# Kernel optimization log

Measured on AMD Instinct MI355X. Metric: run time of the kernel, lower is better.

Reference implementation:

```python
import jax, jax.numpy as jnp
import numpy as np

D_MODEL = 1024
N_HEADS = 16
HEAD_DIM = 64
INNER = N_HEADS * HEAD_DIM
D_FF = 4096


def ln_novar(x, w, b):
    # mean-only 'layernorm' (no variance division), per original LayerNormNoVar
    u = jnp.mean(x, axis=-1, keepdims=True)
    return w * (x - u) + b


def setup_inputs() -> dict:
    key = jax.random.key(0)
    ks = jax.random.split(key, 12)
    s = lambda k, shape, scale: jax.random.normal(k, shape, dtype=jnp.float32) * scale
    inp = {
        "src": s(ks[0], (4, 2048, D_MODEL), 1.0),
        "pre_norm_w": jnp.ones((D_MODEL,), jnp.float32),
        "pre_norm_b": jnp.zeros((D_MODEL,), jnp.float32),
        "wq": s(ks[1], (D_MODEL, INNER), 0.02),
        "wk": s(ks[2], (D_MODEL, INNER), 0.02),
        "wv": s(ks[3], (D_MODEL, INNER), 0.02),
        "w_proj": s(ks[4], (INNER, D_MODEL), 0.02),
        "b_proj": jnp.zeros((D_MODEL,), jnp.float32),
        "norm1_w": jnp.ones((D_MODEL,), jnp.float32),
        "norm1_b": jnp.zeros((D_MODEL,), jnp.float32),
        "w1": s(ks[5], (D_MODEL, D_FF), 0.02),
        "b1": jnp.zeros((D_FF,), jnp.float32),
        "w2": s(ks[6], (D_FF, D_MODEL), 0.02),
        "b2": jnp.zeros((D_MODEL,), jnp.float32),
    }
    return inp


def reference(src, pre_norm_w, pre_norm_b, wq, wk, wv, w_proj, b_proj,
              norm1_w, norm1_b, w1, b1, w2, b2):
    B, N, _ = src.shape
    scale = HEAD_DIM ** -0.5
    x = ln_novar(src, pre_norm_w, pre_norm_b)
    q = (x @ wq).reshape(B, N, N_HEADS, HEAD_DIM)
    k = (x @ wk).reshape(B, N, N_HEADS, HEAD_DIM)
    v = (x @ wv).reshape(B, N, N_HEADS, HEAD_DIM)
    attn = jnp.einsum('bqhd,bkhd->bhqk', q, k) * scale
    attn = jax.nn.softmax(attn, axis=-1)
    o = jnp.einsum('bhqk,bkhd->bqhd', attn, v).reshape(B, N, INNER)
    o = o @ w_proj + b_proj
    src = src + o
    src = ln_novar(src, norm1_w, norm1_b)
    ff = jax.nn.relu(src @ w1 + b1) @ w2 + b2
    return src + ff
```

## Files before the change

### kernel.cpp

```cpp
#include <hip/hip_runtime.h>
#include <hip/hip_bf16.h>
#include <stdint.h>

typedef __hip_bfloat16 bf16;
typedef float f32x4 __attribute__((ext_vector_type(4)));
typedef float f32x16 __attribute__((ext_vector_type(16)));
typedef short v8s __attribute__((ext_vector_type(8)));
typedef __bf16 v8bf __attribute__((ext_vector_type(8)));
typedef unsigned int v4u __attribute__((ext_vector_type(4)));
typedef unsigned int u32;

static constexpr int MROWS = 8192;
static constexpr int DM    = 1024;
static constexpr int DFF   = 4096;
static constexpr int SEQ   = 2048;

__device__ __forceinline__ f32x4 mfma16(v8s a, v8s b, f32x4 c) {
  return __builtin_amdgcn_mfma_f32_16x16x32_bf16(
      __builtin_bit_cast(v8bf, a), __builtin_bit_cast(v8bf, b), c, 0, 0, 0);
}
__device__ __forceinline__ f32x16 mfma32(v8s a, v8s b, f32x16 c) {
  return __builtin_amdgcn_mfma_f32_32x32x16_bf16(
      __builtin_bit_cast(v8bf, a), __builtin_bit_cast(v8bf, b), c, 0, 0, 0);
}

__device__ __forceinline__ void gload_lds16(const void* g, void* l) {
  __builtin_amdgcn_global_load_lds(
      (const __attribute__((address_space(1))) void*)g,
      (__attribute__((address_space(3))) void*)l, 16, 0, 0);
}

__device__ __forceinline__ u32 cvtpk_bf16(float a, float b) {
  u32 r;
  asm("v_cvt_pk_bf16_f32 %0, %1, %2" : "=v"(r) : "v"(a), "v"(b));
  return r;
}
__device__ __forceinline__ void pl32swap(u32& x, u32& y) {
  asm volatile("v_permlane32_swap_b32 %0, %1" : "+v"(x), "+v"(y));
}
__device__ __forceinline__ float fast_exp2(float x) {
  float r;
  asm("v_exp_f32 %0, %1" : "=v"(r) : "v"(x));
  return r;
}

__global__ __launch_bounds__(256) void transpose_cast(
    const float* __restrict__ W, bf16* __restrict__ WT, int K, int N) {
  __shared__ float tile[32][33];
  const int c0 = blockIdx.x * 32;
  const int r0 = blockIdx.y * 32;
  const int tx = threadIdx.x & 31, ty = threadIdx.x >> 5;
  #pragma unroll
  for (int i = 0; i < 32; i += 8)
    tile[ty + i][tx] = W[(size_t)(r0 + ty + i) * N + c0 + tx];
  __syncthreads();
  #pragma unroll
  for (int i = 0; i < 32; i += 8)
    WT[(size_t)(c0 + ty + i) * K + r0 + tx] = __float2bfloat16(tile[tx][ty + i]);
}

__global__ __launch_bounds__(256) void ln_novar_kernel(
    const float* __restrict__ x, const float* __restrict__ w,
    const float* __restrict__ b, bf16* __restrict__ ob, float* __restrict__ of) {
  const int row = blockIdx.x;
  const int t = threadIdx.x;
  const float4 v = ((const float4*)(x + (size_t)row * DM))[t];
  float s = v.x + v.y + v.z + v.w;
  #pragma unroll
  for (int off = 32; off > 0; off >>= 1) s += __shfl_down(s, off, 64);
  __shared__ float wsum[4];
  if ((t & 63) == 0) wsum[t >> 6] = s;
  __syncthreads();
  const float u = (wsum[0] + wsum[1] + wsum[2] + wsum[3]) * (1.0f / DM);
  const float4 wv = ((const float4*)w)[t];
  const float4 bv = ((const float4*)b)[t];
  const float o0 = wv.x * (v.x - u) + bv.x;
  const float o1 = wv.y * (v.y - u) + bv.y;
  const float o2 = wv.z * (v.z - u) + bv.z;
  const float o3 = wv.w * (v.w - u) + bv.w;
  bf16* op = ob + (size_t)row * DM + t * 4;
  op[0] = __float2bfloat16(o0); op[1] = __float2bfloat16(o1);
  op[2] = __float2bfloat16(o2); op[3] = __float2bfloat16(o3);
  if (of) {
    float4 o4; o4.x = o0; o4.y = o1; o4.z = o2; o4.w = o3;
    ((float4*)(of + (size_t)row * DM))[t] = o4;
  }
}

#define BM 128
#define BN 128
#define BK 64
template <int EPI>
__global__ __launch_bounds__(256) void gemm_bt(
    const bf16* __restrict__ A, const bf16* __restrict__ BT,
    bf16* __restrict__ Cb, float* __restrict__ Cf,
    const float* __restrict__ bias, const float* __restrict__ res,
    int M, int Nn, int K) {
  __shared__ __align__(16) bf16 As[2][BM * BK];
  __shared__ __align__(16) bf16 Bs[2][BN * BK];

  const int tid = threadIdx.x;
  const int lane = tid & 63;
  const int wave = tid >> 6;
  const int wr = wave >> 1, wc = wave & 1;

  const int nwg = gridDim.x;
  const int nbx = Nn / BN;
  int bid = (blockIdx.x & 7) * (nwg >> 3) + (blockIdx.x >> 3);
  const int GM = 4;
  const int grp = bid / (GM * nbx);
  const int rem = bid - grp * (GM * nbx);
  const int by = grp * GM + (rem & (GM - 1));
  const int bx = rem >> 2;
  const int tM = by * BM, tN = bx * BN;

  f32x4 acc[4][4] = {};
  const int nk = K / BK;

  auto STAGE = [&](int buf, int kt) {
    const int k0 = kt * BK;
    #pragma unroll
    for (int c = 0; c < 4; ++c) {
      const int slot = tid + c * 256;
      const int row = slot >> 3, s = slot & 7;
      const int kk = ((s ^ (row & 7)) << 3);
      gload_lds16(A + (size_t)(tM + row) * K + k0 + kk, (void*)(&As[buf][0] + slot * 8));
      gload_lds16(BT + (size_t)(tN + row) * K + k0 + kk, (void*)(&Bs[buf][0] + slot * 8));
    }
  };

  STAGE(0, 0);
  asm volatile("s_waitcnt vmcnt(0)" ::: "memory");
  __builtin_amdgcn_s_barrier();
  asm volatile("" ::: "memory");

  for (int kt = 0; kt < nk; ++kt) {
    const int cur = kt & 1;
    if (kt + 1 < nk) STAGE(cur ^ 1, kt + 1);

    #pragma unroll
    for (int kk = 0; kk < 2; ++kk) {
      const int kslot = kk * 4 + (lane >> 4);
      v8s af[4], bfr[4];
      #pragma unroll
      for (int m = 0; m < 4; ++m) {
        const int row = wr * 64 + m * 16 + (lane & 15);
        af[m] = *(const v8s*)(&As[cur][0] + (row * 8 + (kslot ^ (row & 7))) * 8);
      }
      #pragma unroll
      for (int n = 0; n < 4; ++n) {
        const int row = wc * 64 + n * 16 + (lane & 15);
        bfr[n] = *(const v8s*)(&Bs[cur][0] + (row * 8 + (kslot ^ (row & 7))) * 8);
      }
      #pragma unroll
      for (int m = 0; m < 4; ++m)
        #pragma unroll
        for (int n = 0; n < 4; ++n)
          acc[m][n] = mfma16(af[m], bfr[n], acc[m][n]);
    }

    asm volatile("s_waitcnt vmcnt(0)" ::: "memory");
    __builtin_amdgcn_s_barrier();
    asm volatile("" ::: "memory");
  }

  #pragma unroll
  for (int m = 0; m < 4; ++m) {
    #pragma unroll
    for (int n = 0; n < 4; ++n) {
      const int row0 = tM + wr * 64 + m * 16 + ((lane >> 4) << 2);
      const int col = tN + wc * 64 + n * 16 + (lane & 15);
      #pragma unroll
      for (int r = 0; r < 4; ++r) {
        const size_t idx = (size_t)(row0 + r) * Nn + col;
        float v = acc[m][n][r];
        if (EPI == 0) {
          Cb[idx] = __float2bfloat16(v);
        } else if (EPI == 1) {
          v += bias[col];
          v = fmaxf(v, 0.0f);
          Cb[idx] = __float2bfloat16(v);
        } else {
          v += bias[col] + res[idx];
          Cf[idx] = v;
        }
      }
    }
  }
}

__global__ __launch_bounds__(256) void repack_kv(
    const bf16* __restrict__ qkv, bf16* __restrict__ krep,
    bf16* __restrict__ vrep) {
  const int bhkt = blockIdx.x;
  const int bh = bhkt >> 5, kt = bhkt & 31;
  const int b = bh >> 4, h = bh & 15;
  const size_t obase = (size_t)bhkt * 4096;
  #pragma unroll
  for (int it = 0; it < 16; ++it) {
    const int o = it * 256 + threadIdx.x;
    const int ch = o >> 9, rowi = (o >> 3) & 63, e = o & 7;
    krep[obase + o] =
        qkv[(size_t)(b * SEQ + kt * 64 + rowi) * 3072 + 1024 + h * 64 + ch * 8 + e];
    vrep[obase + o] =
        qkv[(size_t)(b * SEQ + kt * 64 + ch * 8 + e) * 3072 + 2048 + h * 64 + rowi];
  }
}

#define PPV(i) ((i) < 16 ? s0[(i) & 15] : s1[(i) & 15])
__global__ __launch_bounds__(256, 4) void attn_kernel(
    const bf16* __restrict__ qkv, const bf16* __restrict__ krep,
    const bf16* __restrict__ vrep, bf16* __restrict__ ob) {
  const int qt = blockIdx.x & 15;
  const int bh = blockIdx.x >> 4;
  const int b = bh >> 4, h = bh & 15;
  const int tid = threadIdx.x;
  const int lane = tid & 63, wave = tid >> 6;
  const int c = lane & 31, hi = lane >> 5;
  const float CEXP = 0.180336880111120426f;

  __shared__ __align__(16) bf16 Ks[2][4096];
  __shared__ __align__(16) bf16 Vs[2][4096];

  const int qrow = qt * 128 + wave * 32 + c;
  const bf16* qp = qkv + (size_t)(b * SEQ + qrow) * 3072 + h * 64;
  v8s qf[4];
  #pragma unroll
  for (int ks = 0; ks < 4; ++ks)
    qf[ks] = *(const v8s*)(qp + ks * 16 + hi * 8);

  f32x16 o0 = {}, o1 = {};
  float mrow = -1e30f, lrow = 0.0f;

  const size_t tilebase = (size_t)(bh * 32) * 4096;
  #pragma unroll
  for (int j = 0; j < 2; ++j) {
    gload_lds16(krep + tilebase + (tid + j * 256) * 8, &Ks[0][(tid + j * 256) * 8]);
    gload_lds16(vrep + tilebase + (tid + j * 256) * 8, &Vs[0][(tid + j * 256) * 8]);
  }
  asm volatile("s_waitcnt vmcnt(0)" ::: "memory");
  __builtin_amdgcn_s_barrier();
  asm volatile("" ::: "memory");

  for (int kt = 0; kt < 32; ++kt) {
    const int cur = kt & 1;
    if (kt < 31) {
      const size_t nb = tilebase + (size_t)(kt + 1) * 4096;
      #pragma unroll
      for (int j = 0; j < 2; ++j) {
        gload_lds16(krep + nb + (tid + j * 256) * 8, &Ks[cur ^ 1][(tid + j * 256) * 8]);
        gload_lds16(vrep + nb + (tid + j * 256) * 8, &Vs[cur ^ 1][(tid + j * 256) * 8]);
      }
    }
    const bf16* KB = Ks[cur];
    const bf16* VB = Vs[cur];

    f32x16 s0 = {}, s1 = {};
    __builtin_amdgcn_s_setprio(1);
    #pragma unroll
    for (int ks = 0; ks < 4; ++ks) {
      const int ch = (2 * ks + hi) * 512;
      v8s a0 = *(const v8s*)(KB + ch + c * 8);
      v8s a1 = *(const v8s*)(KB + ch + (c + 32) * 8);
      s0 = mfma32(a0, qf[ks], s0);
      s1 = mfma32(a1, qf[ks], s1);
    }
    __builtin_amdgcn_s_setprio(0);

    float mA = -1e30f, mB = -1e30f;
    #pragma unroll
    for (int i = 0; i < 16; i += 2) {
      mA = fmaxf(fmaxf(s0[i], s0[i + 1]), mA);
      mB = fmaxf(fmaxf(s1[i], s1[i + 1]), mB);
    }
    float tmax = fmaxf(mA, mB);
    tmax = fmaxf(tmax, __shfl_xor(tmax, 32, 64));
    if (__any(tmax - mrow > 64.0f)) {
      const float mnew = fmaxf(mrow, tmax);
      const float ef = fast_exp2((mrow - mnew) * CEXP);
      mrow = mnew;
      lrow *= ef;
      #pragma unroll
      for (int r = 0; r < 16; ++r) {
        const float efq = __shfl(ef, (r & 3) + 8 * (r >> 2) + 4 * hi, 64);
        o0[r] *= efq;
        o1[r] *= efq;
      }
    }
    const float nmc = -mrow * CEXP;
    float rs0 = 0.0f, rs1 = 0.0f;
    #pragma unroll
    for (int i = 0; i < 16; ++i) {
      s0[i] = fast_exp2(fmaf(s0[i], CEXP, nmc));
      s1[i] = fast_exp2(fmaf(s1[i], CEXP, nmc));
      rs0 += s0[i];
      rs1 += s1[i];
    }
    float rs = rs0 + rs1;
    rs += __shfl_xor(rs, 32, 64);
    lrow += rs;

    v8s pa[4];
    #pragma unroll
    for (int ks = 0; ks < 4; ++ks) {
      u32 x  = cvtpk_bf16(PPV(8 * ks + 0), PPV(8 * ks + 1));
      u32 y  = cvtpk_bf16(PPV(8 * ks + 4), PPV(8 * ks + 5));
      u32 x2 = cvtpk_bf16(PPV(8 * ks + 2), PPV(8 * ks + 3));
      u32 y2 = cvtpk_bf16(PPV(8 * ks + 6), PPV(8 * ks + 7));
      pl32swap(x, y);
      pl32swap(x2, y2);
      v4u w; w.x = x; w.y = x2; w.z = y; w.w = y2;
      pa[ks] = __builtin_bit_cast(v8s, w);
    }

    __builtin_amdgcn_s_setprio(1);
    #pragma unroll
    for (int ks = 0; ks < 4; ++ks) {
      const int ch = (2 * ks + hi) * 512;
      v8s b0 = *(const v8s*)(VB + ch + c * 8);
      v8s b1 = *(const v8s*)(VB + ch + (c + 32) * 8);
      o0 = mfma32(pa[ks], b0, o0);
      o1 = mfma32(pa[ks], b1, o1);
    }
    __builtin_amdgcn_s_setprio(0);

    asm volatile("s_waitcnt vmcnt(0)" ::: "memory");
    __builtin_amdgcn_s_barrier();
    asm volatile("" ::: "memory");
  }

  const float rl = 1.0f / lrow;
  const size_t orow0 = (size_t)(b * SEQ + qt * 128 + wave * 32);
  #pragma unroll
  for (int r = 0; r < 16; ++r) {
    const int q = (r & 3) + 8 * (r >> 2) + 4 * hi;
    const float rq = __shfl(rl, q, 64);
    bf16* op = ob + (orow0 + q) * DM + h * 64;
    op[c] = __float2bfloat16(o0[r] * rq);
    op[32 + c] = __float2bfloat16(o1[r] * rq);
  }
}

extern "C" void kernel_launch(void* const* d_in, const int* in_sizes, int n_in,
                              void* d_out, int out_size, void* d_ws,
                              size_t ws_size, hipStream_t stream) {
  const float* src   = (const float*)d_in[0];
  const float* pnw   = (const float*)d_in[1];
  const float* pnb   = (const float*)d_in[2];
  const float* wq    = (const float*)d_in[3];
  const float* wk    = (const float*)d_in[4];
  const float* wv    = (const float*)d_in[5];
  const float* wproj = (const float*)d_in[6];
  const float* bproj = (const float*)d_in[7];
  const float* n1w   = (const float*)d_in[8];
  const float* n1b   = (const float*)d_in[9];
  const float* w1    = (const float*)d_in[10];
  const float* b1    = (const float*)d_in[11];
  const float* w2    = (const float*)d_in[12];
  const float* b2    = (const float*)d_in[13];
  float* out = (float*)d_out;

  char* ws = (char*)d_ws;
  size_t off = 0;
  bf16* WTqkv = (bf16*)(ws + off); off += (size_t)3072 * 1024 * 2;
  bf16* WTprj = (bf16*)(ws + off); off += (size_t)1024 * 1024 * 2;
  bf16* WT1   = (bf16*)(ws + off); off += (size_t)4096 * 1024 * 2;
  bf16* WT2   = (bf16*)(ws + off); off += (size_t)1024 * 4096 * 2;
  bf16* xb    = (bf16*)(ws + off); off += (size_t)MROWS * DM * 2;
  bf16* qkvb  = (bf16*)(ws + off); off += (size_t)MROWS * 3072 * 2;
  bf16* obuf  = (bf16*)(ws + off); off += (size_t)MROWS * DM * 2;
  float* yf   = (float*)(ws + off); off += (size_t)MROWS * DM * 4;
  bf16* h1    = (bf16*)(ws + off); off += (size_t)MROWS * DFF * 2;
  bf16* krep = h1;
  bf16* vrep = h1 + (size_t)64 * SEQ * 64;

  const dim3 blk(256);

  transpose_cast<<<dim3(32, 32), blk, 0, stream>>>(wq, WTqkv, 1024, 1024);
  transpose_cast<<<dim3(32, 32), blk, 0, stream>>>(wk, WTqkv + 1024 * 1024, 1024, 1024);
  transpose_cast<<<dim3(32, 32), blk, 0, stream>>>(wv, WTqkv + 2048 * 1024, 1024, 1024);
  transpose_cast<<<dim3(32, 32), blk, 0, stream>>>(wproj, WTprj, 1024, 1024);
  transpose_cast<<<dim3(128, 32), blk, 0, stream>>>(w1, WT1, 1024, 4096);
  transpose_cast<<<dim3(32, 128), blk, 0, stream>>>(w2, WT2, 4096, 1024);

  ln_novar_kernel<<<MROWS, blk, 0, stream>>>(src, pnw, pnb, xb, nullptr);

  gemm_bt<0><<<dim3((3072 / BN) * (MROWS / BM)), blk, 0, stream>>>(
      xb, WTqkv, qkvb, nullptr, nullptr, nullptr, MROWS, 3072, 1024);

  repack_kv<<<dim3(64 * 32), blk, 0, stream>>>(qkvb, krep, vrep);

  attn_kernel<<<dim3(16 * 64), dim3(256), 0, stream>>>(qkvb, krep, vrep, obuf);

  gemm_bt<2><<<dim3((1024 / BN) * (MROWS / BM)), blk, 0, stream>>>(
      obuf, WTprj, nullptr, yf, bproj, src, MROWS, 1024, 1024);

  ln_novar_kernel<<<MROWS, blk, 0, stream>>>(yf, n1w, n1b, xb, out);

  gemm_bt<1><<<dim3((4096 / BN) * (MROWS / BM)), blk, 0, stream>>>(
      xb, WT1, h1, nullptr, b1, nullptr, MROWS, 4096, 1024);

  gemm_bt<2><<<dim3((1024 / BN) * (MROWS / BM)), blk, 0, stream>>>(
      h1, WT2, nullptr, out, b2, out, MROWS, 1024, 4096);
}
```

Measured before the change: 426.5 us.

## Triple-buffer GEMM LDS pipeline with 256x128 tiles and 512-thread blocks

Doubles the GEMM M-tile to 256 rows and runs 8 waves per block. It replaces the double-buffered LDS ring with a three-stage ring that prefetches two k-tiles ahead. Partial vmcnt waits let the next stages' loads stay in flight while the current stage is consumed. MFMA bursts are wrapped in s_setprio raises, and the per-tile B reuse roughly doubles. The cost is about 147KB of LDS per block, which limits occupancy to one block per CU, and fewer workgroups per GEMM, which may hurt tail balance on the smaller N=1024 projections.

```diff
diff --git a/kernel.cpp b/kernel.cpp
--- a/kernel.cpp
+++ b/kernel.cpp
@@ -87,17 +87,18 @@
   }
 }
 
-#define BM 128
+#define BM 256
 #define BN 128
 #define BK 64
+#define ASZ (BM * BK)
+#define BSZ (BN * BK)
 template <int EPI>
-__global__ __launch_bounds__(256) void gemm_bt(
+__global__ __launch_bounds__(512) void gemm_bt(
     const bf16* __restrict__ A, const bf16* __restrict__ BT,
     bf16* __restrict__ Cb, float* __restrict__ Cf,
     const float* __restrict__ bias, const float* __restrict__ res,
     int M, int Nn, int K) {
-  __shared__ __align__(16) bf16 As[2][BM * BK];
-  __shared__ __align__(16) bf16 Bs[2][BN * BK];
+  __shared__ __align__(16) bf16 S[3][ASZ + BSZ];
 
   const int tid = threadIdx.x;
   const int lane = tid & 63;
@@ -119,25 +120,39 @@
 
   auto STAGE = [&](int buf, int kt) {
     const int k0 = kt * BK;
+    bf16* Ab = &S[buf][0];
+    bf16* Bb = &S[buf][ASZ];
     #pragma unroll
     for (int c = 0; c < 4; ++c) {
-      const int slot = tid + c * 256;
+      const int slot = c * 512 + tid;
       const int row = slot >> 3, s = slot & 7;
       const int kk = ((s ^ (row & 7)) << 3);
-      gload_lds16(A + (size_t)(tM + row) * K + k0 + kk, (void*)(&As[buf][0] + slot * 8));
-      gload_lds16(BT + (size_t)(tN + row) * K + k0 + kk, (void*)(&Bs[buf][0] + slot * 8));
+      gload_lds16(A + (size_t)(tM + row) * K + k0 + kk, (void*)(Ab + slot * 8));
+    }
+    #pragma unroll
+    for (int c = 0; c < 2; ++c) {
+      const int slot = c * 512 + tid;
+      const int row = slot >> 3, s = slot & 7;
+      const int kk = ((s ^ (row & 7)) << 3);
+      gload_lds16(BT + (size_t)(tN + row) * K + k0 + kk, (void*)(Bb + slot * 8));
     }
   };
 
   STAGE(0, 0);
-  asm volatile("s_waitcnt vmcnt(0)" ::: "memory");
-  __builtin_amdgcn_s_barrier();
-  asm volatile("" ::: "memory");
+  STAGE(1, 1);
 
   for (int kt = 0; kt < nk; ++kt) {
-    const int cur = kt & 1;
-    if (kt + 1 < nk) STAGE(cur ^ 1, kt + 1);
-
+    const int cur = kt % 3;
+    if (kt + 2 < nk) STAGE((kt + 2) % 3, kt + 2);
+
+    if (kt + 2 < nk)      asm volatile("s_waitcnt vmcnt(12)" ::: "memory");
+    else if (kt + 1 < nk) asm volatile("s_waitcnt vmcnt(6)" ::: "memory");
+    else                  asm volatile("s_waitcnt vmcnt(0)" ::: "memory");
+    __builtin_amdgcn_s_barrier();
+    asm volatile("" ::: "memory");
+
+    const bf16* Ab = &S[cur][0];
+    const bf16* Bb = &S[cur][ASZ];
     #pragma unroll
     for (int kk = 0; kk < 2; ++kk) {
       const int kslot = kk * 4 + (lane >> 4);
@@ -145,21 +160,23 @@
       #pragma unroll
       for (int m = 0; m < 4; ++m) {
         const int row = wr * 64 + m * 16 + (lane & 15);
-        af[m] = *(const v8s*)(&As[cur][0] + (row * 8 + (kslot ^ (row & 7))) * 8);
+        af[m] = *(const v8s*)(Ab + (row * 8 + (kslot ^ (row & 7))) * 8);
       }
       #pragma unroll
       for (int n = 0; n < 4; ++n) {
         const int row = wc * 64 + n * 16 + (lane & 15);
-        bfr[n] = *(const v8s*)(&Bs[cur][0] + (row * 8 + (kslot ^ (row & 7))) * 8);
+        bfr[n] = *(const v8s*)(Bb + (row * 8 + (kslot ^ (row & 7))) * 8);
       }
+      __builtin_amdgcn_s_setprio(1);
       #pragma unroll
       for (int m = 0; m < 4; ++m)
         #pragma unroll
         for (int n = 0; n < 4; ++n)
           acc[m][n] = mfma16(af[m], bfr[n], acc[m][n]);
-    }
-
-    asm volatile("s_waitcnt vmcnt(0)" ::: "memory");
+      __builtin_amdgcn_s_setprio(0);
+    }
+
+    asm volatile("" ::: "memory");
     __builtin_amdgcn_s_barrier();
     asm volatile("" ::: "memory");
   }
@@ -375,6 +392,7 @@
   bf16* vrep = h1 + (size_t)64 * SEQ * 64;
 
   const dim3 blk(256);
+  const dim3 gblk(512);
 
   transpose_cast<<<dim3(32, 32), blk, 0, stream>>>(wq, WTqkv, 1024, 1024);
   transpose_cast<<<dim3(32, 32), blk, 0, stream>>>(wk, WTqkv + 1024 * 1024, 1024, 1024);
@@ -385,21 +403,21 @@
 
   ln_novar_kernel<<<MROWS, blk, 0, stream>>>(src, pnw, pnb, xb, nullptr);
 
-  gemm_bt<0><<<dim3((3072 / BN) * (MROWS / BM)), blk, 0, stream>>>(
+  gemm_bt<0><<<dim3((3072 / BN) * (MROWS / BM)), gblk, 0, stream>>>(
       xb, WTqkv, qkvb, nullptr, nullptr, nullptr, MROWS, 3072, 1024);
 
   repack_kv<<<dim3(64 * 32), blk, 0, stream>>>(qkvb, krep, vrep);
 
   attn_kernel<<<dim3(16 * 64), dim3(256), 0, stream>>>(qkvb, krep, vrep, obuf);
 
-  gemm_bt<2><<<dim3((1024 / BN) * (MROWS / BM)), blk, 0, stream>>>(
+  gemm_bt<2><<<dim3((1024 / BN) * (MROWS / BM)), gblk, 0, stream>>>(
       obuf, WTprj, nullptr, yf, bproj, src, MROWS, 1024, 1024);
 
   ln_novar_kernel<<<MROWS, blk, 0, stream>>>(yf, n1w, n1b, xb, out);
 
-  gemm_bt<1><<<dim3((4096 / BN) * (MROWS / BM)), blk, 0, stream>>>(
+  gemm_bt<1><<<dim3((4096 / BN) * (MROWS / BM)), gblk, 0, stream>>>(
       xb, WT1, h1, nullptr, b1, nullptr, MROWS, 4096, 1024);
 
-  gemm_bt<2><<<dim3((1024 / BN) * (MROWS / BM)), blk, 0, stream>>>(
+  gemm_bt<2><<<dim3((1024 / BN) * (MROWS / BM)), gblk, 0, stream>>>(
       h1, WT2, nullptr, out, b2, out, MROWS, 1024, 4096);
 }
```

Result: no change. 428.6 us (+0.5%).
